# Performance work log

Measured on AMD Instinct MI355X. Metric: run time of the kernel, lower is better.

The kernel has to match this reference:

```python
import jax, jax.numpy as jnp
import numpy as np

D_MODEL = 2048
SLOTS = 8
D_FIELD = 256  # SLOTS * D_FIELD == proj output dim == 2048
BATCH = 2
SEQ = 4096


def setup_inputs() -> dict:
    key = jax.random.key(0)
    k1, k2 = jax.random.split(key, 2)
    x = jax.random.normal(k1, (BATCH, SEQ, D_MODEL), dtype=jnp.float32)
    # nn.Linear(d_model, slots*d_field): weight [out, in], bias [out]
    W = jax.random.normal(k2, (SLOTS * D_FIELD, D_MODEL), dtype=jnp.float32) * (1.0 / np.sqrt(D_MODEL))
    b = jnp.zeros((SLOTS * D_FIELD,), dtype=jnp.float32)
    horizons = jnp.array([1., 2., 4., 8., 16., 32., 64., 128.], dtype=jnp.float32)
    alphas = jnp.exp(-1.0 / horizons)  # per-slot EMA decay, length SLOTS
    return {"x": x, "W": W, "b": b, "alphas": alphas}


def reference(x, W, b, alphas):
    B, S, _ = x.shape
    # projection: [B,S,d_model] @ [d_model, slots*d_field] -> [B,S,slots,d_field]
    updates = (jnp.einsum('bsd,od->bso', x, W) + b).reshape(B, S, SLOTS, D_FIELD)
    # linear recurrence state_t = alpha * state_{t-1} + u_t, state_0 = 0,
    # via log-depth associative scan with elements (a_t, u_t)
    a = jnp.broadcast_to(alphas[None, None, :, None], updates.shape)

    def combine(c1, c2):
        a1, u1 = c1
        a2, u2 = c2
        return (a1 * a2, a2 * u1 + u2)

    _, state = jax.lax.associative_scan(combine, (a, updates), axis=1)
    return state  # [B,S,slots,d_field]
```

## Files before the change

### kernel.cpp

```cpp
#include <hip/hip_runtime.h>
#include <hip/hip_bf16.h>
#include <stdint.h>
#include <stddef.h>

#define D_MODEL 2048
#define NOUT    2048
#define BATCH   2
#define SEQ     4096
#define M_TOTAL (BATCH*SEQ)
#define SLOTS   8
#define D_FIELD 256
#define CHUNK   32
#define NCHUNK  (SEQ/CHUNK)
#define NT      (D_MODEL/64)

typedef __attribute__((ext_vector_type(4))) float  floatx4;
typedef __attribute__((ext_vector_type(8))) __bf16 bf16x8;
typedef __attribute__((ext_vector_type(4))) __bf16 bf16x4;

__device__ __forceinline__ void async_copy16(const void* gsrc, void* ldst) {
  __builtin_amdgcn_global_load_lds(
      (__attribute__((address_space(1))) const void*)(uintptr_t)gsrc,
      (__attribute__((address_space(3))) void*)(uintptr_t)ldst,
      16, 0, 0);
}

__global__ void cast_kernel(const float* __restrict__ x,
                            const float* __restrict__ W,
                            __bf16* __restrict__ xb,
                            __bf16* __restrict__ wb) {
  const long long nx = (long long)M_TOTAL * D_MODEL;
  const long long nw = (long long)NOUT * D_MODEL;
  long long base = ((long long)blockIdx.x * blockDim.x + threadIdx.x) * 4;
  if (base < nx) {
    float4 v = *(const float4*)(x + base);
    bf16x4 o;
    o[0] = (__bf16)v.x; o[1] = (__bf16)v.y; o[2] = (__bf16)v.z; o[3] = (__bf16)v.w;
    *(bf16x4*)(xb + base) = o;
  } else {
    long long j = base - nx;
    if (j < nw) {
      float4 v = *(const float4*)(W + j);
      bf16x4 o;
      o[0] = (__bf16)v.x; o[1] = (__bf16)v.y; o[2] = (__bf16)v.z; o[3] = (__bf16)v.w;
      *(bf16x4*)(wb + j) = o;
    }
  }
}

#define VMW4 asm volatile("s_waitcnt vmcnt(4)" ::: "memory")
#define VMW2 asm volatile("s_waitcnt vmcnt(2)" ::: "memory")
#define VMW0 asm volatile("s_waitcnt vmcnt(0)" ::: "memory")
#define LGKM0 do{ asm volatile("s_waitcnt lgkmcnt(0)" ::: "memory"); \
                  __builtin_amdgcn_sched_barrier(0); }while(0)
#define BAR do{ __builtin_amdgcn_s_barrier(); __builtin_amdgcn_sched_barrier(0); }while(0)

#define DSRD(off) (*(const bf16x8*)(smem + (off)))

#define STG(GP, ROFF, DSTOFF, KTN) do{ \
  async_copy16((GP) + (ROFF) + (KTN)*64,      smem + (DSTOFF)); \
  async_copy16((GP) + (ROFF) + (KTN)*64 + 32, smem + (DSTOFF) + 1024); }while(0)

#define RD_AF(BUF, MOFF) do{ \
  _Pragma("unroll") for (int i_ = 0; i_ < 4; ++i_){ \
  _Pragma("unroll") for (int k_ = 0; k_ < 2; ++k_){ \
    afr[i_][k_] = DSRD((BUF)*32768 + ((wM8+(MOFF)+i_)*2+k_)*1024 + fragOff); }} }while(0)

#define RD_BF(BUF, NOFF, DST) do{ \
  _Pragma("unroll") for (int j_ = 0; j_ < 2; ++j_){ \
  _Pragma("unroll") for (int k_ = 0; k_ < 2; ++k_){ \
    DST[j_][k_] = DSRD(65536 + (BUF)*32768 + ((wN4+(NOFF)+j_)*2+k_)*1024 + fragOff); }} }while(0)

#define MFMA_Q(AM, AN, BFR) do{ \
  __builtin_amdgcn_s_setprio(1); \
  _Pragma("unroll") for (int i_ = 0; i_ < 4; ++i_){ \
  _Pragma("unroll") for (int j_ = 0; j_ < 2; ++j_){ \
  _Pragma("unroll") for (int k_ = 0; k_ < 2; ++k_){ \
    acc[(AM)+i_][(AN)+j_] = __builtin_amdgcn_mfma_f32_16x16x32_bf16( \
        afr[i_][k_], BFR[j_][k_], acc[(AM)+i_][(AN)+j_], 0, 0, 0); }}} \
  __builtin_amdgcn_s_setprio(0); }while(0)

#define KTILE(BUF, KTN, DO_STG) do{ \
   \
  RD_AF(BUF, 0); \
  RD_BF(BUF, 0, bfr0); \
  if (DO_STG) STG(gA, rA0, ((BUF)^1)*32768 + dA0, KTN); \
  if (DO_STG) { VMW4; } else { VMW2; } \
  BAR; LGKM0; \
  MFMA_Q(0, 0, bfr0); \
   \
  RD_BF(BUF, 2, bfr1); \
  if (DO_STG) STG(gB, rB0, ((BUF)^1)*32768 + dB0, KTN); \
  if (DO_STG) { VMW4; } else { VMW0; } \
  BAR; LGKM0; \
  MFMA_Q(0, 2, bfr1); \
   \
  RD_AF(BUF, 4); \
  if (DO_STG) STG(gB, rB1, ((BUF)^1)*32768 + dB1, KTN); \
  BAR; LGKM0; \
  MFMA_Q(4, 2, bfr1); \
   \
  if (DO_STG) { STG(gA, rA1, ((BUF)^1)*32768 + dA1, KTN); VMW4; } \
  BAR; \
  MFMA_Q(4, 0, bfr0); \
}while(0)

__global__ __launch_bounds__(512, 2) void gemm_scan_kernel(
    const __bf16* __restrict__ A,
    const __bf16* __restrict__ Bw,
    const float*  __restrict__ bias,
    const float*  __restrict__ alphas,
    float* __restrict__ C,
    float* __restrict__ carry) {
  extern __shared__ __align__(16) char smem[];
  const int t    = threadIdx.x;
  const int lane = t & 63;
  const int w    = t >> 6;
  const int wM   = w >> 2;
  const int wN   = w & 3;
  const int m0   = blockIdx.x * 256;
  const int n0   = blockIdx.y * 256;

  const int lq = lane >> 4, lr = lane & 15;
  const int fragOff = (lr*64 + lq*16) ^ (((lr >> 3) & 1) << 5);
  const int wM8 = wM*8, wN4 = wN*4;

  const int lrow = lane >> 2;
  const int lcol = ((lane & 3) * 8) ^ ((lane >> 5) * 16);
  const int srA0 = (w & 3) + ((w >> 2) << 3), srA1 = srA0 + 4;
  const int srB0 = (w & 1) + ((w >> 1) << 2), srB1 = srB0 + 2;
  const __bf16* gA = A  + (size_t)m0 * D_MODEL + lcol;
  const __bf16* gB = Bw + (size_t)n0 * D_MODEL + lcol;
  const int rA0 = (srA0*16 + lrow) * D_MODEL;
  const int rA1 = (srA1*16 + lrow) * D_MODEL;
  const int rB0 = (srB0*16 + lrow) * D_MODEL;
  const int rB1 = (srB1*16 + lrow) * D_MODEL;
  const int dA0 = srA0*2048 + lane*16;
  const int dA1 = srA1*2048 + lane*16;
  const int dB0 = 65536 + srB0*2048 + lane*16;
  const int dB1 = 65536 + srB1*2048 + lane*16;

  floatx4 acc[8][4] = {};
  bf16x8 afr[4][2], bfr0[2][2], bfr1[2][2];

  STG(gA, rA0, dA0, 0);
  STG(gB, rB0, dB0, 0);
  STG(gB, rB1, dB1, 0);
  STG(gA, rA1, dA1, 0);
  VMW4;
  BAR;

#pragma unroll 1
  for (int p = 0; p < 15; ++p) {
    KTILE(0, 2*p+1, true);
    KTILE(1, 2*p+2, true);
  }
  KTILE(0, 31, true);
  KTILE(1, 0, false);

  const int mW0 = m0 + wM*128;
  const int nW0 = n0 + wN*64;
  const float alpha = alphas[nW0 >> 8];
  const float a2 = alpha*alpha;
  const float a4 = a2*a2;
  const float a8 = a4*a4;
  const float a16 = a8*a8;
  float aq = 1.f;
#pragma unroll
  for (int i = 0; i < 3; ++i) if (i < 3 - lq) aq *= a4;
  const int bb = mW0 >> 12;
  const int j0 = (mW0 & (SEQ - 1)) >> 5;

#pragma unroll
  for (int nf = 0; nf < 4; ++nf) {
    const int n = nW0 + nf*16 + lr;
    const float bv = bias[n];
    float tm[8];
#pragma unroll
    for (int mf = 0; mf < 8; ++mf) {
      const int m = mW0 + mf*16 + lq*4;
      const float u0 = acc[mf][nf][0] + bv;
      const float u1 = acc[mf][nf][1] + bv;
      const float u2 = acc[mf][nf][2] + bv;
      const float u3 = acc[mf][nf][3] + bv;
      C[(size_t)(m+0)*NOUT + n] = u0;
      C[(size_t)(m+1)*NOUT + n] = u1;
      C[(size_t)(m+2)*NOUT + n] = u2;
      C[(size_t)(m+3)*NOUT + n] = u3;
      tm[mf] = ((u0*alpha + u1)*alpha + u2)*alpha + u3;
    }
#pragma unroll
    for (int c = 0; c < 4; ++c) {
      float s = (tm[2*c]*a16 + tm[2*c+1]) * aq;
      s += __shfl_xor(s, 16, 64);
      s += __shfl_xor(s, 32, 64);
      if (lq == 0)
        carry[((size_t)bb*NCHUNK + j0 + c)*NOUT + n] = s;
    }
  }
}

__global__ void scan_apply(float* __restrict__ U,
                           const float* __restrict__ alphas,
                           const float* __restrict__ carry) {
  const int idx  = blockIdx.x * blockDim.x + threadIdx.x;
  const int c    = idx & (NOUT - 1);
  const int rest = idx >> 11;
  const int j    = rest & (NCHUNK - 1);
  const int b    = rest >> 7;
  const float alpha = alphas[c >> 8];
  float aC = alpha;
#pragma unroll
  for (int i = 0; i < 5; ++i) aC *= aC;

  const float* cb = carry + (size_t)b * NCHUNK * NOUT + c;
  float s = 0.f;
#pragma unroll 8
  for (int jp = 0; jp < j; ++jp)
    s = aC * s + cb[(size_t)jp * NOUT];

  float* p = U + ((size_t)(b * SEQ + j * CHUNK) * NOUT) + c;
#pragma unroll 8
  for (int tt = 0; tt < CHUNK; ++tt) {
    const float v = alpha * s + p[(size_t)tt * NOUT];
    p[(size_t)tt * NOUT] = v;
    s = v;
  }
}

extern "C" void kernel_launch(void* const* d_in, const int* in_sizes, int n_in,
                              void* d_out, int out_size, void* d_ws, size_t ws_size,
                              hipStream_t stream) {
  const float* x      = (const float*)d_in[0];
  const float* W      = (const float*)d_in[1];
  const float* bias   = (const float*)d_in[2];
  const float* alphas = (const float*)d_in[3];
  float* out = (float*)d_out;

  __bf16* xb   = (__bf16*)d_ws;
  __bf16* wb   = (__bf16*)((char*)d_ws + (size_t)M_TOTAL * D_MODEL * 2);
  float* carry = (float*)((char*)d_ws + (size_t)M_TOTAL * D_MODEL * 2
                                       + (size_t)NOUT * D_MODEL * 2);

  {
    const long long total = ((long long)M_TOTAL * D_MODEL + (long long)NOUT * D_MODEL) / 4;
    const int blocks = (int)((total + 255) / 256);
    cast_kernel<<<blocks, 256, 0, stream>>>(x, W, xb, wb);
  }
  {
    dim3 grid(M_TOTAL / 256, NOUT / 256);
    gemm_scan_kernel<<<grid, 512, 131072, stream>>>(xb, wb, bias, alphas, out, carry);
  }
  scan_apply<<<(BATCH * NCHUNK * NOUT) / 256, 256, 0, stream>>>(out, alphas, carry);
}
```

Baseline: 211.0 us.

## Fuse chunked scan apply into GEMM epilogue via per-column inter-block barrier

Removes the separate scan_apply kernel. Each GEMM block publishes its chunk carries, then waits on an atomic counter until all 32 M-blocks of its column group have done the same. It then computes its prefix state from the carries and writes the final scanned output directly from the registers. This avoids writing the raw projection to global memory and then reading and rewriting it, at the cost of a spin-wait that requires all blocks to be co-resident, plus counter resets in the cast kernel.

Measured after the change: 208.4 us. About the same (-1.3%).

```diff
diff --git a/kernel.cpp b/kernel.cpp
--- a/kernel.cpp
+++ b/kernel.cpp
@@ -28,7 +28,10 @@
 __global__ void cast_kernel(const float* __restrict__ x,
                             const float* __restrict__ W,
                             __bf16* __restrict__ xb,
-                            __bf16* __restrict__ wb) {
+                            __bf16* __restrict__ wb,
+                            int* __restrict__ ctr) {
+  if (blockIdx.x == 0 && threadIdx.x < 8)
+    __hip_atomic_store(&ctr[threadIdx.x], 0, __ATOMIC_RELAXED, __HIP_MEMORY_SCOPE_AGENT);
   const long long nx = (long long)M_TOTAL * D_MODEL;
   const long long nw = (long long)NOUT * D_MODEL;
   long long base = ((long long)blockIdx.x * blockDim.x + threadIdx.x) * 4;
@@ -105,13 +108,16 @@
   MFMA_Q(4, 0, bfr0); \
 }while(0)
 
+#define CARRY_LD(P) __hip_atomic_load((P), __ATOMIC_RELAXED, __HIP_MEMORY_SCOPE_AGENT)
+
 __global__ __launch_bounds__(512, 2) void gemm_scan_kernel(
     const __bf16* __restrict__ A,
     const __bf16* __restrict__ Bw,
     const float*  __restrict__ bias,
     const float*  __restrict__ alphas,
     float* __restrict__ C,
-    float* __restrict__ carry) {
+    float* __restrict__ carry,
+    int*   __restrict__ ctr) {
   extern __shared__ __align__(16) char smem[];
   const int t    = threadIdx.x;
   const int lane = t & 63;
@@ -161,70 +167,101 @@
   const int mW0 = m0 + wM*128;
   const int nW0 = n0 + wN*64;
   const float alpha = alphas[nW0 >> 8];
-  const float a2 = alpha*alpha;
-  const float a4 = a2*a2;
-  const float a8 = a4*a4;
-  const float a16 = a8*a8;
+  const float a2 = alpha*alpha, a4 = a2*a2, a8 = a4*a4, a16 = a8*a8, a32 = a16*a16;
   float aq = 1.f;
 #pragma unroll
   for (int i = 0; i < 3; ++i) if (i < 3 - lq) aq *= a4;
-  const int bb = mW0 >> 12;
-  const int j0 = (mW0 & (SEQ - 1)) >> 5;
-
+  float a4p = 1.f;
+#pragma unroll
+  for (int i = 0; i < 3; ++i) if (i < lq) a4p *= a4;
+  const int bb  = mW0 >> 12;
+  const int j0w = (mW0 & (SEQ - 1)) >> 5;
+  float* cbase = carry + (size_t)bb * NCHUNK * NOUT;
+
+  float bvv[4], tmv[4][8];
 #pragma unroll
   for (int nf = 0; nf < 4; ++nf) {
     const int n = nW0 + nf*16 + lr;
-    const float bv = bias[n];
-    float tm[8];
+    bvv[nf] = bias[n];
+    const float bv = bvv[nf];
 #pragma unroll
     for (int mf = 0; mf < 8; ++mf) {
-      const int m = mW0 + mf*16 + lq*4;
-      const float u0 = acc[mf][nf][0] + bv;
-      const float u1 = acc[mf][nf][1] + bv;
-      const float u2 = acc[mf][nf][2] + bv;
-      const float u3 = acc[mf][nf][3] + bv;
-      C[(size_t)(m+0)*NOUT + n] = u0;
-      C[(size_t)(m+1)*NOUT + n] = u1;
-      C[(size_t)(m+2)*NOUT + n] = u2;
-      C[(size_t)(m+3)*NOUT + n] = u3;
-      tm[mf] = ((u0*alpha + u1)*alpha + u2)*alpha + u3;
+      const floatx4 av = acc[mf][nf];
+      tmv[nf][mf] = (((av[0]+bv)*alpha + (av[1]+bv))*alpha + (av[2]+bv))*alpha + (av[3]+bv);
     }
 #pragma unroll
     for (int c = 0; c < 4; ++c) {
-      float s = (tm[2*c]*a16 + tm[2*c+1]) * aq;
+      float s = (tmv[nf][2*c]*a16 + tmv[nf][2*c+1]) * aq;
       s += __shfl_xor(s, 16, 64);
       s += __shfl_xor(s, 32, 64);
       if (lq == 0)
-        carry[((size_t)bb*NCHUNK + j0 + c)*NOUT + n] = s;
-    }
-  }
-}
-
-__global__ void scan_apply(float* __restrict__ U,
-                           const float* __restrict__ alphas,
-                           const float* __restrict__ carry) {
-  const int idx  = blockIdx.x * blockDim.x + threadIdx.x;
-  const int c    = idx & (NOUT - 1);
-  const int rest = idx >> 11;
-  const int j    = rest & (NCHUNK - 1);
-  const int b    = rest >> 7;
-  const float alpha = alphas[c >> 8];
-  float aC = alpha;
-#pragma unroll
-  for (int i = 0; i < 5; ++i) aC *= aC;
-
-  const float* cb = carry + (size_t)b * NCHUNK * NOUT + c;
-  float s = 0.f;
-#pragma unroll 8
-  for (int jp = 0; jp < j; ++jp)
-    s = aC * s + cb[(size_t)jp * NOUT];
-
-  float* p = U + ((size_t)(b * SEQ + j * CHUNK) * NOUT) + c;
-#pragma unroll 8
-  for (int tt = 0; tt < CHUNK; ++tt) {
-    const float v = alpha * s + p[(size_t)tt * NOUT];
-    p[(size_t)tt * NOUT] = v;
-    s = v;
+        __hip_atomic_store(&cbase[(size_t)(j0w + c)*NOUT + n], s,
+                           __ATOMIC_RELAXED, __HIP_MEMORY_SCOPE_AGENT);
+    }
+  }
+
+  __syncthreads();
+  if (t == 0) {
+    __hip_atomic_fetch_add(&ctr[blockIdx.y], 1, __ATOMIC_ACQ_REL, __HIP_MEMORY_SCOPE_AGENT);
+    while (__hip_atomic_load(&ctr[blockIdx.y], __ATOMIC_ACQUIRE, __HIP_MEMORY_SCOPE_AGENT) < 32)
+      __builtin_amdgcn_s_sleep(2);
+  }
+  __syncthreads();
+
+  {
+    const float* cbl = cbase + (nW0 + lq*16 + lr);
+    float H = 0.f;
+#pragma unroll 4
+    for (int jp = 0; jp < j0w; ++jp)
+      H = a32*H + CARRY_LD(&cbl[(size_t)jp*NOUT]);
+    float s0[4];
+#pragma unroll
+    for (int nf = 0; nf < 4; ++nf) s0[nf] = __shfl(H, nf*16 + lr, 64);
+
+#pragma unroll
+    for (int nf = 0; nf < 4; ++nf) {
+      const int n = nW0 + nf*16 + lr;
+      const float bv = bvv[nf];
+      float sp = s0[nf];
+#pragma unroll
+      for (int c = 0; c < 4; ++c) {
+        if (c > 0)
+          sp = a32*sp + CARRY_LD(&cbase[(size_t)(j0w + c - 1)*NOUT + n]);
+        float ulo[4], uhi[4];
+#pragma unroll
+        for (int i = 0; i < 4; ++i) {
+          ulo[i] = acc[2*c][nf][i]   + bv;
+          uhi[i] = acc[2*c+1][nf][i] + bv;
+        }
+        const float Tlo = tmv[nf][2*c];
+        const float Thi = tmv[nf][2*c+1];
+        const float t0  = __shfl(Tlo, lr,      64);
+        const float t1  = __shfl(Tlo, 16 + lr, 64);
+        const float t2  = __shfl(Tlo, 32 + lr, 64);
+        const float t3  = __shfl(Tlo, 48 + lr, 64);
+        const float th0 = __shfl(Thi, lr,      64);
+        const float th1 = __shfl(Thi, 16 + lr, 64);
+        const float th2 = __shfl(Thi, 32 + lr, 64);
+        float h = 0.f;
+        if (lq > 0) h = t0;
+        if (lq > 1) h = h*a4 + t1;
+        if (lq > 2) h = h*a4 + t2;
+        float Slo = a4p*sp + h;
+        const float smid = (((t0*a4 + t1)*a4 + t2)*a4 + t3) + a16*sp;
+        float hh = 0.f;
+        if (lq > 0) hh = th0;
+        if (lq > 1) hh = hh*a4 + th1;
+        if (lq > 2) hh = hh*a4 + th2;
+        float Shi = a4p*smid + hh;
+        const size_t rowb = (size_t)(mW0 + 2*c*16 + lq*4);
+        float s = Slo;
+#pragma unroll
+        for (int i = 0; i < 4; ++i) { s = alpha*s + ulo[i]; C[(rowb + i)*NOUT + n] = s; }
+        s = Shi;
+#pragma unroll
+        for (int i = 0; i < 4; ++i) { s = alpha*s + uhi[i]; C[(rowb + 16 + i)*NOUT + n] = s; }
+      }
+    }
   }
 }
 
@@ -241,15 +278,17 @@
   __bf16* wb   = (__bf16*)((char*)d_ws + (size_t)M_TOTAL * D_MODEL * 2);
   float* carry = (float*)((char*)d_ws + (size_t)M_TOTAL * D_MODEL * 2
                                        + (size_t)NOUT * D_MODEL * 2);
+  int* ctr     = (int*)((char*)d_ws + (size_t)M_TOTAL * D_MODEL * 2
+                                     + (size_t)NOUT * D_MODEL * 2
+                                     + (size_t)BATCH * NCHUNK * NOUT * 4);
 
   {
     const long long total = ((long long)M_TOTAL * D_MODEL + (long long)NOUT * D_MODEL) / 4;
     const int blocks = (int)((total + 255) / 256);
-    cast_kernel<<<blocks, 256, 0, stream>>>(x, W, xb, wb);
+    cast_kernel<<<blocks, 256, 0, stream>>>(x, W, xb, wb, ctr);
   }
   {
     dim3 grid(M_TOTAL / 256, NOUT / 256);
-    gemm_scan_kernel<<<grid, 512, 131072, stream>>>(xb, wb, bias, alphas, out, carry);
-  }
-  scan_apply<<<(BATCH * NCHUNK * NOUT) / 256, 256, 0, stream>>>(out, alphas, carry);
-}
+    gemm_scan_kernel<<<grid, 512, 131072, stream>>>(xb, wb, bias, alphas, out, carry, ctr);
+  }
+}
```
